# Kernel optimization log

Hardware: AMD Instinct MI355X
Metric: run time of the kernel (lower is better)

## Reference

```python
import jax, jax.numpy as jnp
import numpy as np

L, B, V, E, H = 128, 64, 10000, 512, 512


def setup_inputs() -> dict:
    key = jax.random.key(0)
    ks = jax.random.split(key, 12)
    s = 0.05
    seq = jax.random.randint(ks[0], (L, B), 0, V, dtype=jnp.int32)
    seq_length = jnp.full((B,), L, dtype=jnp.int32)  # equal lengths -> pack/pad identity
    return {
        "seq": seq,
        "seq_length": seq_length,
        "emb": jax.random.normal(ks[1], (V, E), jnp.float32) * 0.01,  # matches init.normal std=0.01
        "W_ih_f": jax.random.normal(ks[2], (3 * H, E), jnp.float32) * s,
        "W_hh_f": jax.random.normal(ks[3], (3 * H, H), jnp.float32) * s,
        "b_ih_f": jax.random.normal(ks[4], (3 * H,), jnp.float32) * s,
        "b_hh_f": jax.random.normal(ks[5], (3 * H,), jnp.float32) * s,
        "W_ih_b": jax.random.normal(ks[6], (3 * H, E), jnp.float32) * s,
        "W_hh_b": jax.random.normal(ks[7], (3 * H, H), jnp.float32) * s,
        "b_ih_b": jax.random.normal(ks[8], (3 * H,), jnp.float32) * s,
        "b_hh_b": jax.random.normal(ks[9], (3 * H,), jnp.float32) * s,
        "dec_W": jax.random.normal(ks[10], (V, 2 * H), jnp.float32) * s,
        "dec_b": jax.random.normal(ks[11], (V,), jnp.float32) * s,
    }


def _gru(x_emb, W_ih, W_hh, b_ih, b_hh, reverse):
    # x_emb: [L, B, E]; PyTorch GRU cell equations.
    gx = jnp.einsum('lbe,ge->lbg', x_emb, W_ih) + b_ih  # [L, B, 3H]
    h0 = jnp.zeros((x_emb.shape[1], W_hh.shape[1]), x_emb.dtype)

    def step(h, gx_t):
        gh = h @ W_hh.T + b_hh
        r = jax.nn.sigmoid(gx_t[:, :H] + gh[:, :H])
        z = jax.nn.sigmoid(gx_t[:, H:2 * H] + gh[:, H:2 * H])
        n = jnp.tanh(gx_t[:, 2 * H:] + r * gh[:, 2 * H:])
        h_new = (1.0 - z) * n + z * h
        return h_new, h_new

    _, ys = jax.lax.scan(step, h0, gx, reverse=reverse)
    return ys  # [L, B, H], aligned with input positions


def reference(seq, seq_length, emb, W_ih_f, W_hh_f, b_ih_f, b_hh_f,
              W_ih_b, W_hh_b, b_ih_b, b_hh_b, dec_W, dec_b):
    x = emb[seq]  # [L, B, E]; dropout=0 (eval) -> identity
    out_f = _gru(x, W_ih_f, W_hh_f, b_ih_f, b_hh_f, reverse=False)  # [L, B, H]
    out_b = _gru(x, W_ih_b, W_hh_b, b_ih_b, b_hh_b, reverse=True)   # [L, B, H]
    # EditType.REPLACE: fwd state before the edited token, bwd state after it
    out = jnp.concatenate([out_f[0:L - 2], out_b[2:L]], axis=2)  # [L-2, B, 2H]
    logits = jnp.einsum('lbh,vh->lbv', out, dec_W) + dec_b       # [L-2, B, V]
    return jax.nn.log_softmax(logits, axis=-1)
```

## Files before the change

kernel.cpp:

```cpp
#include <hip/hip_runtime.h>
#include <hip/hip_bf16.h>
#include <stdint.h>

#define LL 128
#define BB 64
#define VV 10000
#define EE 512
#define HH 512
#define G3 1536
#define MROWS 8192
#define DM 8064
#define D2H 1024
#define NPAD 10112
#define FP 16
#define NTILE_M 63
#define NTILE_N 79
#define DECQ (NTILE_M * NTILE_N)

typedef __bf16 bf16x8 __attribute__((ext_vector_type(8)));
typedef float f32x4 __attribute__((ext_vector_type(4)));
typedef int i32x4 __attribute__((ext_vector_type(4)));
typedef unsigned int u32x4 __attribute__((ext_vector_type(4)));
typedef unsigned int u32x2 __attribute__((ext_vector_type(2)));
typedef unsigned short u16;
typedef unsigned long long u64;

static __device__ __forceinline__ float bf2f(u16 u) {
  unsigned int x = ((unsigned int)u) << 16;
  return __builtin_bit_cast(float, x);
}
static __device__ __forceinline__ u16 f2bf(float f) {
  unsigned int x = __builtin_bit_cast(unsigned int, f);
  unsigned int r = x + 0x7FFFu + ((x >> 16) & 1u);
  return (u16)(r >> 16);
}
static __device__ __forceinline__ signed char q8(float v) {
  float r = fminf(fmaxf(rintf(v), -127.f), 127.f);
  return (signed char)(int)r;
}

static __device__ __forceinline__ void cstore16(void* p, u32x4 v) {
  asm volatile("global_store_dwordx4 %0, %1, off sc0 sc1" :: "v"(p), "v"(v) : "memory");
}
static __device__ __forceinline__ void cstore8(void* p, u64 v) {
  u32x2 d = __builtin_bit_cast(u32x2, v);
  asm volatile("global_store_dwordx2 %0, %1, off sc0 sc1" :: "v"(p), "v"(d) : "memory");
}
static __device__ __forceinline__ void flagstore4(void* p, int v) {
  asm volatile("global_store_dword %0, %1, off sc0 sc1" :: "v"(p), "v"(v) : "memory");
}
static __device__ __forceinline__ int flagload4(const void* p) {
  int v;
  asm volatile("global_load_dword %0, %1, off sc0 sc1\n\ts_waitcnt vmcnt(0)"
               : "=v"(v) : "v"(p) : "memory");
  return v;
}
static __device__ __forceinline__ void gload_lds16(const void* g, void* s) {
  __builtin_amdgcn_global_load_lds(
      (const __attribute__((address_space(1))) unsigned int*)g,
      (__attribute__((address_space(3))) unsigned int*)s, 16, 0, 0);
}

__global__ __launch_bounds__(256) void k_prep(
    const float* __restrict__ decW, signed char* __restrict__ decWq,
    float* __restrict__ wscale,
    const int* __restrict__ seq, const float* __restrict__ emb,
    u16* __restrict__ xb,
    const float* __restrict__ Whhf, const float* __restrict__ Whhb,
    const float* __restrict__ Wihf, const float* __restrict__ Wihb,
    u16* __restrict__ Whh_bf, u16* __restrict__ Wih_bf)
{
  __shared__ float red[4];
  __shared__ float s_inv;
  const int bid = blockIdx.x;
  const int tid = threadIdx.x;

  if (bid < VV) {
    const int v = bid;
    const int l = tid & 63, w = tid >> 6;
    float4 x = *(const float4*)(decW + (long)v * 1024 + tid * 4);
    float m = fmaxf(fmaxf(fabsf(x.x), fabsf(x.y)), fmaxf(fabsf(x.z), fabsf(x.w)));
#pragma unroll
    for (int off = 32; off; off >>= 1) m = fmaxf(m, __shfl_xor(m, off));
    if (l == 0) red[w] = m;
    __syncthreads();
    if (tid == 0) {
      float mm = fmaxf(fmaxf(red[0], red[1]), fmaxf(red[2], red[3]));
      mm = fmaxf(mm, 1e-12f);
      s_inv = 127.f / mm;
      wscale[v] = mm / (127.f * 127.f);
    }
    __syncthreads();
    float inv = s_inv;
    char4 o;
    o.x = q8(x.x * inv); o.y = q8(x.y * inv); o.z = q8(x.z * inv); o.w = q8(x.w * inv);
    *(char4*)(decWq + (long)v * 1024 + tid * 4) = o;
  } else if (bid < VV + 4096) {
    int rb = (bid - VV) * 2 + (tid >> 7);
    int t = tid & 127;
    int v = seq[rb];
    float4 val = ((const float4*)(emb + (long)v * EE))[t];
    ushort4 o;
    o.x = f2bf(val.x); o.y = f2bf(val.y); o.z = f2bf(val.z); o.w = f2bf(val.w);
    ((ushort4*)(xb + (long)rb * EE))[t] = o;
  } else {
    int c = bid - VV - 4096;
    int tensor = c / 768;
    int i = (c % 768) * 256 + tid;
    const float4* s; ushort4* d;
    switch (tensor) {
      case 0: s = (const float4*)Whhf; d = (ushort4*)Whh_bf; break;
      case 1: s = (const float4*)Whhb; d = (ushort4*)(Whh_bf + G3 * HH); break;
      case 2: s = (const float4*)Wihf; d = (ushort4*)Wih_bf; break;
      default: s = (const float4*)Wihb; d = (ushort4*)(Wih_bf + G3 * EE); break;
    }
    float4 v = s[i];
    ushort4 o;
    o.x = f2bf(v.x); o.y = f2bf(v.y); o.z = f2bf(v.z); o.w = f2bf(v.w);
    d[i] = o;
  }
}

__global__ __launch_bounds__(256) void k_gemm_gx(
    const u16* __restrict__ A, const u16* __restrict__ W0, const u16* __restrict__ W1,
    const float* __restrict__ b0, const float* __restrict__ b1, u16* __restrict__ C)
{
  __shared__ char smem[32768];
  const int tid = threadIdx.x;
  const int l = tid & 63;
  const int w = tid >> 6;
  const int wr = w >> 1, wc = w & 1;
  const long tM = (long)blockIdx.x * 128;
  const long tN = (long)blockIdx.y * 128;
  const int z = blockIdx.z;
  const u16* B = z ? W1 : W0;
  const float* bias = z ? b1 : b0;
  u16* Cz = C + (size_t)z * MROWS * G3;

  f32x4 acc[4][4];
#pragma unroll
  for (int m = 0; m < 4; m++)
#pragma unroll
    for (int n = 0; n < 4; n++) acc[m][n] = {0.f, 0.f, 0.f, 0.f};

  for (int kt = 0; kt < 8; ++kt) {
    const int k0 = kt << 6;
#pragma unroll
    for (int i = 0; i < 4; i++) {
      int cchunk = w * 4 + i;
      int c = cchunk * 64 + l;
      int row = c >> 3, k8 = c & 7;
      gload_lds16(A + (tM + row) * EE + k0 + k8 * 8, smem + cchunk * 1024);
      gload_lds16(B + (tN + row) * EE + k0 + k8 * 8, smem + 16384 + cchunk * 1024);
    }
    __syncthreads();
#pragma unroll
    for (int kk = 0; kk < 2; kk++) {
      const int kb = kk * 64 + ((l >> 4) * 16);
      bf16x8 af[4], bfr[4];
#pragma unroll
      for (int m = 0; m < 4; m++) {
        int ra = wr * 64 + m * 16 + (l & 15);
        af[m] = *(const bf16x8*)(smem + ra * 128 + kb);
      }
#pragma unroll
      for (int n = 0; n < 4; n++) {
        int rb2 = wc * 64 + n * 16 + (l & 15);
        bfr[n] = *(const bf16x8*)(smem + 16384 + rb2 * 128 + kb);
      }
#pragma unroll
      for (int m = 0; m < 4; m++)
#pragma unroll
        for (int n = 0; n < 4; n++)
          acc[m][n] = __builtin_amdgcn_mfma_f32_16x16x32_bf16(af[m], bfr[n], acc[m][n], 0, 0, 0);
    }
    __syncthreads();
  }
#pragma unroll
  for (int n = 0; n < 4; n++) {
    long col = tN + wc * 64 + n * 16 + (l & 15);
    float bv = bias[col];
#pragma unroll
    for (int m = 0; m < 4; m++) {
      long row = tM + wr * 64 + m * 16 + ((l >> 4) * 4);
#pragma unroll
      for (int r = 0; r < 4; r++)
        Cz[(row + r) * G3 + col] = f2bf(acc[m][n][r] + bv);
    }
  }
}

static __device__ void gru_body(
    int blk, int dir, int tid, char* lds,
    const u16* __restrict__ Whh_all,
    const float* __restrict__ bhh_f, const float* __restrict__ bhh_b,
    const u16* __restrict__ gx_all, u16* __restrict__ hsteps,
    signed char* __restrict__ catq, int* __restrict__ bar16)
{
  const int l = tid & 63, w = tid >> 6;
  const u16* Whh = Whh_all + (long)dir * G3 * HH;
  const float* bhh = dir ? bhh_b : bhh_f;
  const u16* gx = gx_all + (long)dir * MROWS * G3;

  char* Wl = lds;
  u16 (*hstage)[32] = (u16(*)[32])(lds + 96 * 1024);
  signed char (*hstageq)[32] = (signed char(*)[32])(lds + 96 * 1024 + 4096);

  for (int c = tid; c < 6144; c += 256) {
    int lr = c >> 6;
    int k8 = c & 63;
    int gr = (lr >> 5) * HH + blk * 32 + (lr & 31);
    uint4 v = *(const uint4*)(Whh + (long)gr * HH + k8 * 8);
    *(uint4*)(Wl + lr * 1024 + ((k8 * 16) ^ ((lr & 7) << 4))) = v;
  }
  float bh[6];
#pragma unroll
  for (int n = 0; n < 6; n++) {
    int c = n * 16 + (l & 15);
    bh[n] = bhh[(c >> 5) * HH + blk * 32 + (c & 31)];
  }
  float hreg[4][2] = {};
  __syncthreads();

  const int lrow = w * 16 + ((l >> 4) * 4);
  const int srow = tid >> 2, schunk = tid & 3;

  u16 gxn[3][4][2];
  {
    const int lpos0 = dir ? (LL - 1) : 0;
#pragma unroll
    for (int r = 0; r < 4; r++) {
      const u16* gxr = gx + ((long)lpos0 * BB + (lrow + r)) * G3 + blk * 32;
#pragma unroll
      for (int g = 0; g < 3; g++)
#pragma unroll
        for (int p = 0; p < 2; p++)
          gxn[g][r][p] = gxr[g * HH + p * 16 + (l & 15)];
    }
  }

  for (int t = 0; t < LL; ++t) {
    const int lpos = dir ? (LL - 1 - t) : t;
    const u16* hsrc = hsteps + ((size_t)t * 2 + dir) * BB * HH;

    u16 gxv[3][4][2];
#pragma unroll
    for (int g = 0; g < 3; g++)
#pragma unroll
      for (int r = 0; r < 4; r++)
#pragma unroll
        for (int p = 0; p < 2; p++) gxv[g][r][p] = gxn[g][r][p];

    bf16x8 af[16];
    {
      const u16* hrow = hsrc + (w * 16 + (l & 15)) * HH + ((l >> 4) * 8);
#pragma unroll
      for (int kc = 0; kc < 16; kc++) af[kc] = *(const bf16x8*)(hrow + kc * 32);
    }

    f32x4 acc[6];
#pragma unroll
    for (int n = 0; n < 6; n++) acc[n] = {0.f, 0.f, 0.f, 0.f};
#pragma unroll
    for (int kc = 0; kc < 16; kc++) {
      const int kb = kc * 64 + ((l >> 4) * 16);
#pragma unroll
      for (int n = 0; n < 6; n++) {
        int lr = n * 16 + (l & 15);
        bf16x8 bfr = *(const bf16x8*)(Wl + lr * 1024 + (kb ^ ((l & 7) << 4)));
        acc[n] = __builtin_amdgcn_mfma_f32_16x16x32_bf16(af[kc], bfr, acc[n], 0, 0, 0);
      }
    }

#pragma unroll
    for (int r = 0; r < 4; r++) {
#pragma unroll
      for (int p = 0; p < 2; p++) {
        float ghr = acc[0 + p][r] + bh[0 + p];
        float ghz = acc[2 + p][r] + bh[2 + p];
        float ghn = acc[4 + p][r] + bh[4 + p];
        float xr = bf2f(gxv[0][r][p]);
        float xz = bf2f(gxv[1][r][p]);
        float xn = bf2f(gxv[2][r][p]);
        float ar = fminf(fmaxf(xr + ghr, -30.f), 30.f);
        float az = fminf(fmaxf(xz + ghz, -30.f), 30.f);
        float rg = 1.f / (1.f + __expf(-ar));
        float zg = 1.f / (1.f + __expf(-az));
        float an = fminf(fmaxf(xn + rg * ghn, -30.f), 30.f);
        float e2 = __expf(-2.f * an);
        float ng = (1.f - e2) / (1.f + e2);
        float hn = (1.f - zg) * ng + zg * hreg[r][p];
        hreg[r][p] = hn;
        hstage[lrow + r][p * 16 + (l & 15)] = f2bf(hn);
        hstageq[lrow + r][p * 16 + (l & 15)] = q8(hn * 127.f);
      }
    }
    __syncthreads();

    u32x4 hv = *(const u32x4*)&hstage[srow][schunk * 8];
    u64 hq = *(const u64*)&hstageq[srow][schunk * 8];
    if (t < LL - 1)
      cstore16(hsteps + ((size_t)(t + 1) * 2 + dir) * BB * HH + srow * HH + blk * 32 + schunk * 8, hv);
    if (dir == 0) {
      if (lpos < LL - 2)
        cstore8(catq + ((long)lpos * BB + srow) * D2H + blk * 32 + schunk * 8, hq);
    } else {
      if (lpos >= 2)
        cstore8(catq + ((long)(lpos - 2) * BB + srow) * D2H + HH + blk * 32 + schunk * 8, hq);
    }
    if (t < LL - 1) {
      asm volatile("s_waitcnt vmcnt(0)" ::: "memory");
      __syncthreads();
      if (tid == 0)
        flagstore4(&bar16[((dir * LL + t) * 16 + blk) * FP], 1);
      {
        const int lposn = dir ? (LL - 2 - t) : (t + 1);
#pragma unroll
        for (int r = 0; r < 4; r++) {
          const u16* gxr = gx + ((long)lposn * BB + (lrow + r)) * G3 + blk * 32;
#pragma unroll
          for (int g = 0; g < 3; g++)
#pragma unroll
            for (int p = 0; p < 2; p++)
              gxn[g][r][p] = gxr[g * HH + p * 16 + (l & 15)];
        }
      }
      const int* flg = bar16 + (dir * LL + t) * 16 * FP;
      for (;;) {
        int v = 1;
        if (l < 16) v = flagload4(&flg[l * FP]);
        if (__all(v != 0)) break;
      }
      __builtin_amdgcn_sched_barrier(0);
    }
  }
}

static __device__ void dec_body(
    int tid, char* smem, int* tk_sh,
    const signed char* __restrict__ A, const signed char* __restrict__ B,
    const float* __restrict__ wscale, const float* __restrict__ bias,
    void* __restrict__ Cv, int outbf,
    int* __restrict__ ticket, const int* __restrict__ bar16)
{
  const int l = tid & 63;
  const int w = tid >> 6;
  const int wr = w >> 1, wc = w & 1;

  for (;;) {
    if (tid == 0)
      *tk_sh = __hip_atomic_fetch_add(ticket, 1, __ATOMIC_RELAXED, __HIP_MEMORY_SCOPE_AGENT);
    __syncthreads();
    const int n = *tk_sh;
    __syncthreads();
    if (n >= DECQ) return;
    const int k = n / NTILE_N, j = n % NTILE_N;
    const int mi = (k & 1) ? (31 + ((k + 1) >> 1)) : (31 - (k >> 1));
    const long tM = (long)mi * 128;
    const long tN = (long)j * 128;

    {
      const int tf = 2 * mi + 1;
      const int tb = 125 - 2 * mi;
      const int* fp = (l < 16)
          ? bar16 + ((0 * LL + tf) * 16 + l) * FP
          : bar16 + ((1 * LL + tb) * 16 + (l & 15)) * FP;
      for (;;) {
        int v = 1;
        if (l < 32) v = flagload4(fp);
        if (__all(v != 0)) break;
      }
    }

    i32x4 acc[4][4];
#pragma unroll
    for (int m = 0; m < 4; m++)
#pragma unroll
      for (int nn = 0; nn < 4; nn++) acc[m][nn] = {0, 0, 0, 0};

    for (int kt = 0; kt < 8; ++kt) {
      const int k0 = kt << 7;
#pragma unroll
      for (int i = 0; i < 4; i++) {
        int jj = w * 4 + i;
        int row = jj * 8 + (l >> 3);
        int k16 = l & 7;
        gload_lds16(A + (tM + row) * 1024 + k0 + k16 * 16, smem + jj * 1024);
        gload_lds16(B + (tN + row) * 1024 + k0 + k16 * 16, smem + 16384 + jj * 1024);
      }
      __syncthreads();
#pragma unroll
      for (int ks = 0; ks < 2; ks++) {
        const int kb = ks * 64 + ((l >> 4) * 16);
        i32x4 af[4], bfr[4];
#pragma unroll
        for (int m = 0; m < 4; m++) {
          int ra = wr * 64 + m * 16 + (l & 15);
          af[m] = *(const i32x4*)(smem + ra * 128 + kb);
        }
#pragma unroll
        for (int nn = 0; nn < 4; nn++) {
          int rb2 = wc * 64 + nn * 16 + (l & 15);
          bfr[nn] = *(const i32x4*)(smem + 16384 + rb2 * 128 + kb);
        }
#pragma unroll
        for (int m = 0; m < 4; m++)
#pragma unroll
          for (int nn = 0; nn < 4; nn++)
            acc[m][nn] = __builtin_amdgcn_mfma_i32_16x16x64_i8(af[m], bfr[nn], acc[m][nn], 0, 0, 0);
      }
      __syncthreads();
    }
#pragma unroll
    for (int nn = 0; nn < 4; nn++) {
      long col = tN + wc * 64 + nn * 16 + (l & 15);
      if (col < VV) {
        float sc = wscale[col];
        float bv = bias[col];
#pragma unroll
        for (int m = 0; m < 4; m++) {
          long row = tM + wr * 64 + m * 16 + ((l >> 4) * 4);
#pragma unroll
          for (int r = 0; r < 4; r++) {
            float vv = (float)acc[m][nn][r] * sc + bv;
            if (outbf) ((u16*)Cv)[(row + r) * NPAD + col] = f2bf(vv);
            else       ((float*)Cv)[(row + r) * VV + col] = vv;
          }
        }
      }
    }
  }
}

__global__ __launch_bounds__(256) void k_fused(
    const u16* __restrict__ Whh_all,
    const float* __restrict__ bhh_f, const float* __restrict__ bhh_b,
    const u16* __restrict__ gx_all, u16* __restrict__ hsteps,
    signed char* __restrict__ catq, int* __restrict__ bar16,
    const signed char* __restrict__ decWq, const float* __restrict__ wscale,
    const float* __restrict__ decb, void* __restrict__ Cv, int outbf,
    int* __restrict__ ticket)
{
  __shared__ __align__(16) char lds[104448];
  __shared__ int tk_sh;
  const int bid = blockIdx.x;
  const int tid = threadIdx.x;
  if (bid < 32) {
    gru_body(bid >> 1, bid & 1, tid, lds, Whh_all, bhh_f, bhh_b, gx_all,
             hsteps, catq, bar16);
  } else {
    dec_body(tid, lds, &tk_sh, catq, decWq, wscale, decb, Cv, outbf, ticket, bar16);
  }
}

__global__ __launch_bounds__(256) void k_lsm(float* __restrict__ out) {
  const long row = blockIdx.x;
  float* p = out + row * VV;
  const int tid = threadIdx.x;
  const int l = tid & 63, w = tid >> 6;
  __shared__ float red[8];

  float4 v[10];
  float m = -1e30f;
#pragma unroll
  for (int j = 0; j < 10; j++) {
    int idx = j * 256 + tid;
    if (idx < 2500) {
      v[j] = *(float4*)(p + idx * 4);
      m = fmaxf(m, fmaxf(fmaxf(v[j].x, v[j].y), fmaxf(v[j].z, v[j].w)));
    }
  }
#pragma unroll
  for (int off = 32; off; off >>= 1) m = fmaxf(m, __shfl_xor(m, off));
  if (l == 0) red[w] = m;
  __syncthreads();
  m = fmaxf(fmaxf(red[0], red[1]), fmaxf(red[2], red[3]));

  float s = 0.f;
#pragma unroll
  for (int j = 0; j < 10; j++) {
    int idx = j * 256 + tid;
    if (idx < 2500) {
      s += __expf(v[j].x - m) + __expf(v[j].y - m) + __expf(v[j].z - m) + __expf(v[j].w - m);
    }
  }
#pragma unroll
  for (int off = 32; off; off >>= 1) s += __shfl_xor(s, off);
  if (l == 0) red[4 + w] = s;
  __syncthreads();
  s = red[4] + red[5] + red[6] + red[7];
  float lse = m + logf(s);

#pragma unroll
  for (int j = 0; j < 10; j++) {
    int idx = j * 256 + tid;
    if (idx < 2500) {
      float4 o;
      o.x = v[j].x - lse; o.y = v[j].y - lse; o.z = v[j].z - lse; o.w = v[j].w - lse;
      *(float4*)(p + idx * 4) = o;
    }
  }
}

__global__ __launch_bounds__(256) void k_lsm_b(const u16* __restrict__ lg,
                                               float* __restrict__ out) {
  const long row = blockIdx.x;
  const u16* p = lg + row * NPAD;
  float* q = out + row * VV;
  const int tid = threadIdx.x;
  const int l = tid & 63, w = tid >> 6;
  __shared__ float red[8];

  float v[5][8];
  float m = -1e30f;
#pragma unroll
  for (int j = 0; j < 5; j++) {
    int idx8 = j * 256 + tid;
    if (idx8 < 1250) {
      u32x4 u = *(const u32x4*)(p + idx8 * 8);
#pragma unroll
      for (int e = 0; e < 4; e++) {
        v[j][2 * e]     = bf2f((u16)(u[e] & 0xffffu));
        v[j][2 * e + 1] = bf2f((u16)(u[e] >> 16));
      }
#pragma unroll
      for (int e = 0; e < 8; e++) m = fmaxf(m, v[j][e]);
    }
  }
#pragma unroll
  for (int off = 32; off; off >>= 1) m = fmaxf(m, __shfl_xor(m, off));
  if (l == 0) red[w] = m;
  __syncthreads();
  m = fmaxf(fmaxf(red[0], red[1]), fmaxf(red[2], red[3]));

  float s = 0.f;
#pragma unroll
  for (int j = 0; j < 5; j++) {
    int idx8 = j * 256 + tid;
    if (idx8 < 1250) {
#pragma unroll
      for (int e = 0; e < 8; e++) s += __expf(v[j][e] - m);
    }
  }
#pragma unroll
  for (int off = 32; off; off >>= 1) s += __shfl_xor(s, off);
  if (l == 0) red[4 + w] = s;
  __syncthreads();
  s = red[4] + red[5] + red[6] + red[7];
  float lse = m + logf(s);

#pragma unroll
  for (int j = 0; j < 5; j++) {
    int idx8 = j * 256 + tid;
    if (idx8 < 1250) {
      float4 a, b;
      a.x = v[j][0] - lse; a.y = v[j][1] - lse; a.z = v[j][2] - lse; a.w = v[j][3] - lse;
      b.x = v[j][4] - lse; b.y = v[j][5] - lse; b.z = v[j][6] - lse; b.w = v[j][7] - lse;
      *(float4*)(q + idx8 * 8) = a;
      *(float4*)(q + idx8 * 8 + 4) = b;
    }
  }
}

extern "C" void kernel_launch(void* const* d_in, const int* in_sizes, int n_in,
                              void* d_out, int out_size, void* d_ws, size_t ws_size,
                              hipStream_t stream) {
  const int*   seq  = (const int*)d_in[0];
  const float* emb  = (const float*)d_in[2];
  const float* Wihf = (const float*)d_in[3];
  const float* Whhf = (const float*)d_in[4];
  const float* bihf = (const float*)d_in[5];
  const float* bhhf = (const float*)d_in[6];
  const float* Wihb = (const float*)d_in[7];
  const float* Whhb = (const float*)d_in[8];
  const float* bihb = (const float*)d_in[9];
  const float* bhhb = (const float*)d_in[10];
  const float* decW = (const float*)d_in[11];
  const float* decb = (const float*)d_in[12];

  char* ws = (char*)d_ws;
  size_t off = 0;
  u16* Whh_bf = (u16*)(ws + off); off += (size_t)2 * G3 * HH * 2;
  u16* Wih_bf = (u16*)(ws + off); off += (size_t)2 * G3 * EE * 2;
  signed char* decWq = (signed char*)(ws + off); off += (size_t)NPAD * 1024;
  float* wscale = (float*)(ws + off); off += (size_t)NPAD * 4;
  u16* xb = (u16*)(ws + off); off += (size_t)MROWS * EE * 2;
  u16* gxb = (u16*)(ws + off); off += (size_t)2 * MROWS * G3 * 2;
  signed char* catq = (signed char*)(ws + off); off += (size_t)DM * D2H;
  u16* hsteps = (u16*)(ws + off); off += (size_t)(LL + 1) * 2 * BB * HH * 2;
  int* bar16 = (int*)(ws + off); off += (size_t)2 * LL * 16 * FP * 4;
  int* ticket = (int*)(ws + off); off += 64;
  u16* logitsb = (u16*)(ws + off);
  const size_t logits_bytes = (size_t)DM * NPAD * 2;
  const bool use_bf16_logits = (ws_size >= off + logits_bytes);

  (void)hipMemsetAsync(hsteps, 0, (size_t)2 * BB * HH * 2, stream);
  (void)hipMemsetAsync(bar16, 0, (size_t)2 * LL * 16 * FP * 4 + 64, stream);

  k_prep<<<dim3(VV + 4096 + 3072), 256, 0, stream>>>(
      decW, decWq, wscale, seq, emb, xb,
      Whhf, Whhb, Wihf, Wihb, Whh_bf, Wih_bf);

  k_gemm_gx<<<dim3(64, 12, 2), 256, 0, stream>>>(xb, Wih_bf, Wih_bf + G3 * EE,
                                                 bihf, bihb, gxb);

  void* Cv = use_bf16_logits ? (void*)logitsb : (void*)d_out;
  k_fused<<<dim3(256), 256, 0, stream>>>(Whh_bf, bhhf, bhhb, gxb, hsteps, catq,
                                         bar16, decWq, wscale, decb, Cv,
                                         use_bf16_logits ? 1 : 0, ticket);

  if (use_bf16_logits) k_lsm_b<<<DM, 256, 0, stream>>>(logitsb, (float*)d_out);
  else                 k_lsm<<<DM, 256, 0, stream>>>((float*)d_out);
}
```

Before: 978.4 us.

## Move decoder weight quantization and W_hh conversion into fused persistent kernel

```diff
diff --git a/kernel.cpp b/kernel.cpp
--- a/kernel.cpp
+++ b/kernel.cpp
@@ -16,6 +16,8 @@
 #define NTILE_M 63
 #define NTILE_N 79
 #define DECQ (NTILE_M * NTILE_N)
+#define DECB 224
+#define QROWS 45
 
 typedef __bf16 bf16x8 __attribute__((ext_vector_type(8)));
 typedef float f32x4 __attribute__((ext_vector_type(4)));
@@ -62,41 +64,15 @@
 }
 
 __global__ __launch_bounds__(256) void k_prep(
-    const float* __restrict__ decW, signed char* __restrict__ decWq,
-    float* __restrict__ wscale,
     const int* __restrict__ seq, const float* __restrict__ emb,
     u16* __restrict__ xb,
-    const float* __restrict__ Whhf, const float* __restrict__ Whhb,
     const float* __restrict__ Wihf, const float* __restrict__ Wihb,
-    u16* __restrict__ Whh_bf, u16* __restrict__ Wih_bf)
+    u16* __restrict__ Wih_bf)
 {
-  __shared__ float red[4];
-  __shared__ float s_inv;
   const int bid = blockIdx.x;
   const int tid = threadIdx.x;
-
-  if (bid < VV) {
-    const int v = bid;
-    const int l = tid & 63, w = tid >> 6;
-    float4 x = *(const float4*)(decW + (long)v * 1024 + tid * 4);
-    float m = fmaxf(fmaxf(fabsf(x.x), fabsf(x.y)), fmaxf(fabsf(x.z), fabsf(x.w)));
-#pragma unroll
-    for (int off = 32; off; off >>= 1) m = fmaxf(m, __shfl_xor(m, off));
-    if (l == 0) red[w] = m;
-    __syncthreads();
-    if (tid == 0) {
-      float mm = fmaxf(fmaxf(red[0], red[1]), fmaxf(red[2], red[3]));
-      mm = fmaxf(mm, 1e-12f);
-      s_inv = 127.f / mm;
-      wscale[v] = mm / (127.f * 127.f);
-    }
-    __syncthreads();
-    float inv = s_inv;
-    char4 o;
-    o.x = q8(x.x * inv); o.y = q8(x.y * inv); o.z = q8(x.z * inv); o.w = q8(x.w * inv);
-    *(char4*)(decWq + (long)v * 1024 + tid * 4) = o;
-  } else if (bid < VV + 4096) {
-    int rb = (bid - VV) * 2 + (tid >> 7);
+  if (bid < 4096) {
+    int rb = bid * 2 + (tid >> 7);
     int t = tid & 127;
     int v = seq[rb];
     float4 val = ((const float4*)(emb + (long)v * EE))[t];
@@ -104,16 +80,11 @@
     o.x = f2bf(val.x); o.y = f2bf(val.y); o.z = f2bf(val.z); o.w = f2bf(val.w);
     ((ushort4*)(xb + (long)rb * EE))[t] = o;
   } else {
-    int c = bid - VV - 4096;
+    int c = bid - 4096;
     int tensor = c / 768;
     int i = (c % 768) * 256 + tid;
-    const float4* s; ushort4* d;
-    switch (tensor) {
-      case 0: s = (const float4*)Whhf; d = (ushort4*)Whh_bf; break;
-      case 1: s = (const float4*)Whhb; d = (ushort4*)(Whh_bf + G3 * HH); break;
-      case 2: s = (const float4*)Wihf; d = (ushort4*)Wih_bf; break;
-      default: s = (const float4*)Wihb; d = (ushort4*)(Wih_bf + G3 * EE); break;
-    }
+    const float4* s = tensor ? (const float4*)Wihb : (const float4*)Wihf;
+    ushort4* d = tensor ? (ushort4*)(Wih_bf + G3 * EE) : (ushort4*)Wih_bf;
     float4 v = s[i];
     ushort4 o;
     o.x = f2bf(v.x); o.y = f2bf(v.y); o.z = f2bf(v.z); o.w = f2bf(v.w);
@@ -190,17 +161,15 @@
   }
 }
 
+
 static __device__ void gru_body(
     int blk, int dir, int tid, char* lds,
-    const u16* __restrict__ Whh_all,
-    const float* __restrict__ bhh_f, const float* __restrict__ bhh_b,
-    const u16* __restrict__ gx_all, u16* __restrict__ hsteps,
+    const float* __restrict__ Whh_f,
+    const float* __restrict__ bhh,
+    const u16* __restrict__ gx, u16* __restrict__ hsteps,
     signed char* __restrict__ catq, int* __restrict__ bar16)
 {
   const int l = tid & 63, w = tid >> 6;
-  const u16* Whh = Whh_all + (long)dir * G3 * HH;
-  const float* bhh = dir ? bhh_b : bhh_f;
-  const u16* gx = gx_all + (long)dir * MROWS * G3;
 
   char* Wl = lds;
   u16 (*hstage)[32] = (u16(*)[32])(lds + 96 * 1024);
@@ -210,8 +179,15 @@
     int lr = c >> 6;
     int k8 = c & 63;
     int gr = (lr >> 5) * HH + blk * 32 + (lr & 31);
-    uint4 v = *(const uint4*)(Whh + (long)gr * HH + k8 * 8);
-    *(uint4*)(Wl + lr * 1024 + ((k8 * 16) ^ ((lr & 7) << 4))) = v;
+    const float* src = Whh_f + (long)gr * HH + k8 * 8;
+    float4 a = *(const float4*)src;
+    float4 b = *(const float4*)(src + 4);
+    u32x4 packed;
+    packed[0] = ((unsigned)f2bf(a.y) << 16) | f2bf(a.x);
+    packed[1] = ((unsigned)f2bf(a.w) << 16) | f2bf(a.z);
+    packed[2] = ((unsigned)f2bf(b.y) << 16) | f2bf(b.x);
+    packed[3] = ((unsigned)f2bf(b.w) << 16) | f2bf(b.z);
+    *(u32x4*)(Wl + lr * 1024 + ((k8 * 16) ^ ((lr & 7) << 4))) = packed;
   }
   float bh[6];
 #pragma unroll
@@ -337,15 +313,48 @@
 }
 
 static __device__ void dec_body(
-    int tid, char* smem, int* tk_sh,
-    const signed char* __restrict__ A, const signed char* __restrict__ B,
-    const float* __restrict__ wscale, const float* __restrict__ bias,
+    int wid, int tid, char* smem, int* tk_sh,
+    const float* __restrict__ decW, signed char* __restrict__ decWq,
+    float* __restrict__ wscale,
+    const signed char* __restrict__ A,
+    const float* __restrict__ bias,
     void* __restrict__ Cv, int outbf,
-    int* __restrict__ ticket, const int* __restrict__ bar16)
+    int* __restrict__ ticket, const int* __restrict__ bar16,
+    int* __restrict__ prep_done)
 {
   const int l = tid & 63;
   const int w = tid >> 6;
   const int wr = w >> 1, wc = w & 1;
+  float* red = (float*)smem;
+
+  {
+    const int r0 = wid * QROWS;
+    const int r1 = (r0 + QROWS < VV) ? r0 + QROWS : VV;
+    for (int v = r0; v < r1; ++v) {
+      float4 x = *(const float4*)(decW + (long)v * 1024 + tid * 4);
+      float m = fmaxf(fmaxf(fabsf(x.x), fabsf(x.y)), fmaxf(fabsf(x.z), fabsf(x.w)));
+#pragma unroll
+      for (int off = 32; off; off >>= 1) m = fmaxf(m, __shfl_xor(m, off));
+      if (l == 0) red[w] = m;
+      __syncthreads();
+      float mm = fmaxf(fmaxf(red[0], red[1]), fmaxf(red[2], red[3]));
+      mm = fmaxf(mm, 1e-12f);
+      __syncthreads();
+      float inv = 127.f / mm;
+      if (tid == 0) wscale[v] = mm / (127.f * 127.f);
+      char4 o;
+      o.x = q8(x.x * inv); o.y = q8(x.y * inv); o.z = q8(x.z * inv); o.w = q8(x.w * inv);
+      *(char4*)(decWq + (long)v * 1024 + tid * 4) = o;
+    }
+    asm volatile("s_waitcnt vmcnt(0)" ::: "memory");
+    __syncthreads();
+    if (tid == 0) {
+      __hip_atomic_fetch_add(prep_done, 1, __ATOMIC_RELEASE, __HIP_MEMORY_SCOPE_AGENT);
+      while (__hip_atomic_load(prep_done, __ATOMIC_ACQUIRE, __HIP_MEMORY_SCOPE_AGENT) < DECB)
+        __builtin_amdgcn_s_sleep(2);
+    }
+    __syncthreads();
+  }
 
   for (;;) {
     if (tid == 0)
@@ -386,7 +395,7 @@
         int row = jj * 8 + (l >> 3);
         int k16 = l & 7;
         gload_lds16(A + (tM + row) * 1024 + k0 + k16 * 16, smem + jj * 1024);
-        gload_lds16(B + (tN + row) * 1024 + k0 + k16 * 16, smem + 16384 + jj * 1024);
+        gload_lds16(decWq + (tN + row) * 1024 + k0 + k16 * 16, smem + 16384 + jj * 1024);
       }
       __syncthreads();
 #pragma unroll
@@ -433,11 +442,12 @@
 }
 
 __global__ __launch_bounds__(256) void k_fused(
-    const u16* __restrict__ Whh_all,
+    const float* __restrict__ Whhf, const float* __restrict__ Whhb,
     const float* __restrict__ bhh_f, const float* __restrict__ bhh_b,
     const u16* __restrict__ gx_all, u16* __restrict__ hsteps,
     signed char* __restrict__ catq, int* __restrict__ bar16,
-    const signed char* __restrict__ decWq, const float* __restrict__ wscale,
+    const float* __restrict__ decW, signed char* __restrict__ decWq,
+    float* __restrict__ wscale,
     const float* __restrict__ decb, void* __restrict__ Cv, int outbf,
     int* __restrict__ ticket)
 {
@@ -446,10 +456,13 @@
   const int bid = blockIdx.x;
   const int tid = threadIdx.x;
   if (bid < 32) {
-    gru_body(bid >> 1, bid & 1, tid, lds, Whh_all, bhh_f, bhh_b, gx_all,
-             hsteps, catq, bar16);
+    const int dir = bid & 1;
+    gru_body(bid >> 1, dir, tid, lds,
+             dir ? Whhb : Whhf, dir ? bhh_b : bhh_f,
+             gx_all + (size_t)dir * MROWS * G3, hsteps, catq, bar16);
   } else {
-    dec_body(tid, lds, &tk_sh, catq, decWq, wscale, decb, Cv, outbf, ticket, bar16);
+    dec_body(bid - 32, tid, lds, &tk_sh, decW, decWq, wscale, catq, decb,
+             Cv, outbf, ticket, bar16, ticket + 8);
   }
 }
 
@@ -580,7 +593,6 @@
 
   char* ws = (char*)d_ws;
   size_t off = 0;
-  u16* Whh_bf = (u16*)(ws + off); off += (size_t)2 * G3 * HH * 2;
   u16* Wih_bf = (u16*)(ws + off); off += (size_t)2 * G3 * EE * 2;
   signed char* decWq = (signed char*)(ws + off); off += (size_t)NPAD * 1024;
   float* wscale = (float*)(ws + off); off += (size_t)NPAD * 4;
@@ -597,17 +609,16 @@
   (void)hipMemsetAsync(hsteps, 0, (size_t)2 * BB * HH * 2, stream);
   (void)hipMemsetAsync(bar16, 0, (size_t)2 * LL * 16 * FP * 4 + 64, stream);
 
-  k_prep<<<dim3(VV + 4096 + 3072), 256, 0, stream>>>(
-      decW, decWq, wscale, seq, emb, xb,
-      Whhf, Whhb, Wihf, Wihb, Whh_bf, Wih_bf);
+  k_prep<<<dim3(4096 + 1536), 256, 0, stream>>>(seq, emb, xb, Wihf, Wihb, Wih_bf);
 
   k_gemm_gx<<<dim3(64, 12, 2), 256, 0, stream>>>(xb, Wih_bf, Wih_bf + G3 * EE,
                                                  bihf, bihb, gxb);
 
   void* Cv = use_bf16_logits ? (void*)logitsb : (void*)d_out;
-  k_fused<<<dim3(256), 256, 0, stream>>>(Whh_bf, bhhf, bhhb, gxb, hsteps, catq,
-                                         bar16, decWq, wscale, decb, Cv,
-                                         use_bf16_logits ? 1 : 0, ticket);
+  k_fused<<<dim3(256), 256, 0, stream>>>(Whhf, Whhb, bhhf, bhhb, gxb, hsteps,
+                                         catq, bar16, decW, decWq, wscale,
+                                         decb, Cv, use_bf16_logits ? 1 : 0,
+                                         ticket);
 
   if (use_bf16_logits) k_lsm_b<<<DM, 256, 0, stream>>>(logitsb, (float*)d_out);
   else                 k_lsm<<<DM, 256, 0, stream>>>((float*)d_out);
```

After: 991.8 us. No clear change (+1.4%).
